# Optimization experiments

Hardware: AMD Instinct MI355X
Metric: run time of the kernel (lower is better)

## Reference

```python
import jax, jax.numpy as jnp
import numpy as np
from jax import lax

T, I, H, L = 4096, 101, 1000, 4  # seq len, letters_num, hidden, num_layers


def setup_inputs() -> dict:
    key = jax.random.key(0)
    ks = jax.random.split(key, 9)
    s = 0.03  # weight scale ~ 1/sqrt(H)
    return {
        "x": jax.random.normal(ks[0], (T, 1, I), jnp.float32),
        "enc_Wih": jax.random.normal(ks[1], (L, 4 * H, I), jnp.float32) * s,
        "enc_Whh": jax.random.normal(ks[2], (L, 4 * H, H), jnp.float32) * s,
        "enc_bih": jax.random.normal(ks[3], (L, 4 * H), jnp.float32) * s,
        "enc_bhh": jax.random.normal(ks[4], (L, 4 * H), jnp.float32) * s,
        "dec_Wih": jax.random.normal(ks[5], (L, 4 * I, H), jnp.float32) * s,
        "dec_Whh": jax.random.normal(ks[6], (L, 4 * I, I), jnp.float32) * s,
        "dec_bih": jax.random.normal(ks[7], (L, 4 * I), jnp.float32) * s,
        "dec_bhh": jax.random.normal(ks[8], (L, 4 * I), jnp.float32) * s,
        "length": T,
    }


def _lstm_cell(x, h, c, Wih, Whh, bih, bhh):
    # PyTorch LSTMCell gate order: i, f, g, o
    gates = x @ Wih.T + bih + h @ Whh.T + bhh  # [T, 4*Hout]
    i, f, g, o = jnp.split(gates, 4, axis=-1)
    c = jax.nn.sigmoid(f) * c + jax.nn.sigmoid(i) * jnp.tanh(g)
    h = jax.nn.sigmoid(o) * jnp.tanh(c)
    return h, c


def _stack(xt, Wih, Whh, bih, bhh, hout):
    # Hidden is reset per timestep in the original, so timesteps are a batch;
    # only the layer chain is sequential. Every layer consumes the same xt.
    t = xt.shape[0]
    init = (jnp.zeros((t, hout), xt.dtype), jnp.zeros((t, hout), xt.dtype))

    def body(carry, p):
        h, c = carry
        wih, whh, bi, bh = p
        h, c = _lstm_cell(xt, h, c, wih, whh, bi, bh)
        return (h, c), None

    (h, _), _ = lax.scan(body, init, (Wih, Whh, bih, bhh))
    return h


def reference(x, enc_Wih, enc_Whh, enc_bih, enc_bhh,
              dec_Wih, dec_Whh, dec_bih, dec_bhh, length):
    xt = x[:, 0, :]                      # [T, I]
    hdim = enc_Whh.shape[-1]
    odim = dec_Whh.shape[-1]
    enc = jax.nn.relu(_stack(xt, enc_Wih, enc_Whh, enc_bih, enc_bhh, hdim))  # [T, H]
    dec = _stack(enc, dec_Wih, dec_Whh, dec_bih, dec_bhh, odim)              # [T, O]
    out = jax.nn.log_softmax(dec, axis=-1)[:, None, :]                       # [T, 1, O]
    return out
```

## Files before the change

kernel.cpp:

```cpp
#include <hip/hip_runtime.h>
#include <cstdint>
#include <cstddef>
#include <cmath>

typedef __bf16 bf16_t;
typedef __bf16 bf16x8 __attribute__((ext_vector_type(8)));
typedef float floatx4 __attribute__((ext_vector_type(4)));

#define AS1 __attribute__((address_space(1)))
#define AS3 __attribute__((address_space(3)))

__device__ __forceinline__ void gload_lds16(const bf16_t* g, bf16_t* l) {
    __builtin_amdgcn_global_load_lds((AS1 void*)(uintptr_t)(g), (AS3 void*)(l), 16, 0, 0);
}

__device__ __forceinline__ float sigf(float x) { return 1.0f / (1.0f + __expf(-x)); }
__device__ __forceinline__ float tanhfast(float x) { return 1.0f - 2.0f / (__expf(2.0f * x) + 1.0f); }

template<int BM>
__global__ __launch_bounds__(256, 4)
void gemm_lstm(const bf16_t* __restrict__ A, const bf16_t* __restrict__ B,
               const float* __restrict__ bias,
               const float* __restrict__ zp, float* __restrict__ zout, int ldZ,
               float* __restrict__ c, int EP,
               bf16_t* __restrict__ hb, int ldH, int hoff, float* __restrict__ hf,
               int K, int ldA, int ldB, int relu, int czero)
{
    constexpr int AI = BM / 32;
    __shared__ bf16_t As[BM * 64];
    __shared__ bf16_t Bs[128 * 64];
    const int tid  = threadIdx.x;
    const int lane = tid & 63;
    const int w    = tid >> 6;
    const int wm   = (w & 1) * (BM / 2);
    const int wn   = (w >> 1) * 64;
    const int m0   = blockIdx.y * BM;
    const int n0   = blockIdx.x * 128;

    floatx4 zero = {0.0f, 0.0f, 0.0f, 0.0f};
    floatx4 acc[AI][4];
#pragma unroll
    for (int i = 0; i < AI; ++i)
#pragma unroll
        for (int j = 0; j < 4; ++j) acc[i][j] = zero;

    const int srow = lane >> 3;
    const int sk   = ((lane & 7) ^ srow) * 8;
    const int fr   = lane & 15;
    const int fx   = fr & 7;

    const bf16_t* Ag = A + (size_t)(m0 + srow) * ldA + sk;
    const bf16_t* Bg = B + (size_t)(n0 + srow) * ldB + sk;

    for (int k0 = 0; k0 < K; k0 += 64) {
        __syncthreads();
#pragma unroll
        for (int j = 0; j < AI; ++j) {
            int r0 = (w * AI + j) * 8;
            gload_lds16(Ag + (size_t)r0 * ldA + k0, As + r0 * 64 + lane * 8);
        }
#pragma unroll
        for (int j = 0; j < 4; ++j) {
            int r0 = (w * 4 + j) * 8;
            gload_lds16(Bg + (size_t)r0 * ldB + k0, Bs + r0 * 64 + lane * 8);
        }
        __syncthreads();
#pragma unroll
        for (int kk = 0; kk < 64; kk += 32) {
            const int pc = ((((kk >> 3) + (lane >> 4)) ^ fx) << 3);
            bf16x8 af[AI], bfr[4];
#pragma unroll
            for (int i = 0; i < AI; ++i)
                af[i] = *(const bf16x8*)(As + (wm + i * 16 + fr) * 64 + pc);
#pragma unroll
            for (int j = 0; j < 4; ++j)
                bfr[j] = *(const bf16x8*)(Bs + (wn + j * 16 + fr) * 64 + pc);
#pragma unroll
            for (int i = 0; i < AI; ++i)
#pragma unroll
                for (int j = 0; j < 4; ++j)
                    acc[i][j] = __builtin_amdgcn_mfma_f32_16x16x32_bf16(af[i], bfr[j], acc[i][j], 0, 0, 0);
        }
    }

    const int crow = (lane >> 4) * 4;
    const int ccol = lane & 15;
    const int nn   = n0 + wn;

    if (zout) {
        float bi[4];
#pragma unroll
        for (int j = 0; j < 4; ++j) bi[j] = bias[nn + j * 16 + ccol];
#pragma unroll
        for (int i = 0; i < AI; ++i) {
#pragma unroll
            for (int r = 0; r < 4; ++r) {
                int t = m0 + wm + i * 16 + crow + r;
                float* zr = zout + (size_t)t * ldZ + nn + ccol;
#pragma unroll
                for (int j = 0; j < 4; ++j) zr[j * 16] = acc[i][j][r] + bi[j];
            }
        }
        return;
    }

    const int e = (nn >> 2) + ccol;
    float bi[4];
    if (!zp) {
#pragma unroll
        for (int j = 0; j < 4; ++j) bi[j] = bias[nn + j * 16 + ccol];
    }

#pragma unroll
    for (int i = 0; i < AI; ++i) {
#pragma unroll
        for (int r = 0; r < 4; ++r) {
            int t = m0 + wm + i * 16 + crow + r;
            float g0, g1, g2, g3;
            if (zp) {
                const float* zr = zp + (size_t)t * ldZ + nn + ccol;
                g0 = acc[i][0][r] + zr[0];
                g1 = acc[i][1][r] + zr[16];
                g2 = acc[i][2][r] + zr[32];
                g3 = acc[i][3][r] + zr[48];
            } else {
                g0 = acc[i][0][r] + bi[0];
                g1 = acc[i][1][r] + bi[1];
                g2 = acc[i][2][r] + bi[2];
                g3 = acc[i][3][r] + bi[3];
            }
            size_t cix = (size_t)t * EP + e;
            float cold = 0.0f;
            if (!czero) cold = c[cix];
            float cv = sigf(g1) * cold + sigf(g0) * tanhfast(g2);
            c[cix] = cv;
            float hv = sigf(g3) * tanhfast(cv);
            if (relu) hv = fmaxf(hv, 0.0f);
            if (hb) hb[(size_t)t * ldH + hoff + e] = (bf16_t)hv;
            else    hf[(size_t)t * EP + e] = hv;
        }
    }
}

__global__ void pack_all(const float* __restrict__ x,
                         const float* __restrict__ eWih, const float* __restrict__ eWhh,
                         const float* __restrict__ ebih, const float* __restrict__ ebhh,
                         const float* __restrict__ dWih, const float* __restrict__ dWhh,
                         const float* __restrict__ dbih, const float* __restrict__ dbhh,
                         bf16_t* __restrict__ Aenc, bf16_t* __restrict__ Wenc,
                         bf16_t* __restrict__ Wdec,
                         float* __restrict__ bse, float* __restrict__ bsd)
{
    const int b = blockIdx.x;
    if (b < 9216) {
        int gid = b * 256 + threadIdx.x;
        int row = gid / 144, grp = gid - row * 144;
        int l = row >> 12, p = row & 4095;
        int g = (p >> 4) & 3, e = ((p >> 6) << 4) + (p & 15);
        int c0 = grp * 8;
        float v[8];
#pragma unroll
        for (int u = 0; u < 8; ++u) v[u] = 0.0f;
        if (e < 1000) {
            size_t r = (size_t)l * 4000 + g * 1000 + e;
            if (c0 >= 128 && c0 < 1128) {
                const float* src = eWhh + r * 1000 + (c0 - 128);
                float4 a = *(const float4*)src;
                float4 bq = *(const float4*)(src + 4);
                v[0]=a.x; v[1]=a.y; v[2]=a.z; v[3]=a.w; v[4]=bq.x; v[5]=bq.y; v[6]=bq.z; v[7]=bq.w;
            } else if (c0 < 128) {
                const float* src = eWih + r * 101;
#pragma unroll
                for (int u = 0; u < 8; ++u) { int cc = c0 + u; if (cc < 101) v[u] = src[cc]; }
            }
        }
        bf16x8 o;
#pragma unroll
        for (int u = 0; u < 8; ++u) o[u] = (bf16_t)v[u];
        *(bf16x8*)(Wenc + (size_t)row * 1152 + c0) = o;
    } else if (b < 11520) {
        int gid = (b - 9216) * 256 + threadIdx.x;
        int row = gid / 144, grp = gid - row * 144;
        int c0  = grp * 8;
        float v[8];
#pragma unroll
        for (int u = 0; u < 8; ++u) v[u] = 0.0f;
        if (c0 < 101) {
            const float* src = x + (size_t)row * 101;
#pragma unroll
            for (int u = 0; u < 8; ++u) { int cc = c0 + u; if (cc < 101) v[u] = src[cc]; }
        }
        bf16x8 o;
#pragma unroll
        for (int u = 0; u < 8; ++u) o[u] = (bf16_t)v[u];
        *(bf16x8*)(Aenc + (size_t)row * 1152 + c0) = o;
    } else if (b < 12672) {
        int gid = (b - 11520) * 256 + threadIdx.x;
        int row = gid / 144, grp = gid - row * 144;
        int l = row >> 9, p = row & 511;
        int g = (p >> 4) & 3, e = ((p >> 6) << 4) + (p & 15);
        int c0 = grp * 8;
        float v[8];
#pragma unroll
        for (int u = 0; u < 8; ++u) v[u] = 0.0f;
        if (e < 101) {
            size_t r = (size_t)l * 404 + g * 101 + e;
            if (c0 < 1000) {
                const float* src = dWih + r * 1000 + c0;
                float4 a = *(const float4*)src;
                float4 bq = *(const float4*)(src + 4);
                v[0]=a.x; v[1]=a.y; v[2]=a.z; v[3]=a.w; v[4]=bq.x; v[5]=bq.y; v[6]=bq.z; v[7]=bq.w;
            } else if (c0 >= 1024 && c0 < 1128) {
                const float* src = dWhh + r * 101;
#pragma unroll
                for (int u = 0; u < 8; ++u) { int cc = c0 + u; if (cc < 1125) v[u] = src[cc - 1024]; }
            }
        }
        bf16x8 o;
#pragma unroll
        for (int u = 0; u < 8; ++u) o[u] = (bf16_t)v[u];
        *(bf16x8*)(Wdec + (size_t)row * 1152 + c0) = o;
    } else {
        int idx = (b - 12672) * 256 + threadIdx.x;
        if (idx < 16384) {
            int l = idx >> 12, p = idx & 4095;
            int g = (p >> 4) & 3, e = ((p >> 6) << 4) + (p & 15);
            bse[idx] = (e < 1000) ? (ebih[l * 4000 + g * 1000 + e] + ebhh[l * 4000 + g * 1000 + e]) : 0.0f;
        } else {
            int k = idx - 16384;
            int l = k >> 9, p = k & 511;
            int g = (p >> 4) & 3, e = ((p >> 6) << 4) + (p & 15);
            bsd[k] = (e < 101) ? (dbih[l * 404 + g * 101 + e] + dbhh[l * 404 + g * 101 + e]) : 0.0f;
        }
    }
}

__global__ void log_softmax_k(const float* __restrict__ h, float* __restrict__ out)
{
    int row = blockIdx.x;
    int l   = threadIdx.x;
    const float* hr = h + (size_t)row * 128;
    float v1 = (l < 101)      ? hr[l]      : -INFINITY;
    float v2 = (l + 64 < 101) ? hr[l + 64] : -INFINITY;
    float m = fmaxf(v1, v2);
#pragma unroll
    for (int off = 32; off > 0; off >>= 1) m = fmaxf(m, __shfl_down(m, off));
    m = __shfl(m, 0);
    float ev = ((l < 101) ? __expf(v1 - m) : 0.0f) + ((l + 64 < 101) ? __expf(v2 - m) : 0.0f);
#pragma unroll
    for (int off = 32; off > 0; off >>= 1) ev += __shfl_down(ev, off);
    float lse = m + __logf(__shfl(ev, 0));
    float* orow = out + (size_t)row * 101;
    if (l < 101)      orow[l]      = v1 - lse;
    if (l + 64 < 101) orow[l + 64] = v2 - lse;
}

extern "C" void kernel_launch(void* const* d_in, const int* in_sizes, int n_in,
                              void* d_out, int out_size, void* d_ws, size_t ws_size,
                              hipStream_t stream)
{
    (void)in_sizes; (void)n_in; (void)out_size; (void)ws_size;
    const float* x    = (const float*)d_in[0];
    const float* eWih = (const float*)d_in[1];
    const float* eWhh = (const float*)d_in[2];
    const float* ebih = (const float*)d_in[3];
    const float* ebhh = (const float*)d_in[4];
    const float* dWih = (const float*)d_in[5];
    const float* dWhh = (const float*)d_in[6];
    const float* dbih = (const float*)d_in[7];
    const float* dbhh = (const float*)d_in[8];

    char* ws = (char*)d_ws;
    bf16_t* Aenc = (bf16_t*)(ws);
    bf16_t* Wenc = (bf16_t*)(ws + 9437184);
    bf16_t* Adec = (bf16_t*)(ws + 47185920);
    bf16_t* Wdec = (bf16_t*)(ws + 56623104);
    float*  bse  = (float*) (ws + 61341696);
    float*  bsd  = (float*) (ws + 61407232);
    float*  cenc = (float*) (ws + 61415424);
    float*  cdec = (float*) (ws + 78192640);
    float*  hdec = (float*) (ws + 80289792);
    float*  Z    = (float*)(ws + 9437184);

    pack_all<<<12744, 256, 0, stream>>>(x, eWih, eWhh, ebih, ebhh, dWih, dWhh, dbih, dbhh,
                                        Aenc, Wenc, Wdec, bse, bsd);

    for (int l = 0; l < 4; ++l) {
        gemm_lstm<128><<<dim3(32, 32), 256, 0, stream>>>(
            Aenc, Wenc + (size_t)l * 4096 * 1152, bse + l * 4096,
            nullptr, nullptr, 0,
            cenc, 1024,
            (l < 3) ? Aenc : Adec, 1152, (l < 3) ? 128 : 0, nullptr,
            (l == 0) ? 128 : 1152, 1152, 1152, (l == 3) ? 1 : 0, (l == 0) ? 1 : 0);
    }

    gemm_lstm<128><<<dim3(16, 32), 256, 0, stream>>>(
        Adec, Wdec, bsd,
        nullptr, Z, 2048,
        nullptr, 0,
        nullptr, 0, 0, nullptr,
        1024, 1152, 1152, 0, 0);

    for (int l = 0; l < 4; ++l) {
        gemm_lstm<32><<<dim3(4, 128), 256, 0, stream>>>(
            Adec + 1024, Wdec + 1024, bsd + l * 512,
            Z + l * 512, nullptr, 2048,
            cdec, 128,
            (l < 3) ? Adec : nullptr, 1152, 1024, (l == 3) ? hdec : nullptr,
            (l == 0) ? 0 : 128, 1152, 1152, 0, (l == 0) ? 1 : 0);
    }
    log_softmax_k<<<4096, 64, 0, stream>>>(hdec, (float*)d_out);
}
```

Measured before the change: 339.3 us.

## Fuse decoder LSTM layers and log-softmax into a single kernel

Replaces the four per-layer decoder GEMM+LSTM launches and the separate log_softmax launch with one kernel. Each block handles 16 timesteps across all four decoder layers. The cell state stays in registers and the hidden state in LDS, and log-softmax runs at the end. This removes launch overhead and the global-memory traffic for c and h between layers. The cost is low parallelism (256 blocks) and recurrent weights read directly from global memory without LDS staging.

```diff
diff --git a/kernel.cpp b/kernel.cpp
--- a/kernel.cpp
+++ b/kernel.cpp
@@ -21,9 +21,9 @@
 __global__ __launch_bounds__(256, 4)
 void gemm_lstm(const bf16_t* __restrict__ A, const bf16_t* __restrict__ B,
                const float* __restrict__ bias,
-               const float* __restrict__ zp, float* __restrict__ zout, int ldZ,
+               float* __restrict__ zout, int ldZ,
                float* __restrict__ c, int EP,
-               bf16_t* __restrict__ hb, int ldH, int hoff, float* __restrict__ hf,
+               bf16_t* __restrict__ hb, int ldH, int hoff,
                int K, int ldA, int ldB, int relu, int czero)
 {
     constexpr int AI = BM / 32;
@@ -86,11 +86,11 @@
     const int crow = (lane >> 4) * 4;
     const int ccol = lane & 15;
     const int nn   = n0 + wn;
+    float bi[4];
+#pragma unroll
+    for (int j = 0; j < 4; ++j) bi[j] = bias[nn + j * 16 + ccol];
 
     if (zout) {
-        float bi[4];
-#pragma unroll
-        for (int j = 0; j < 4; ++j) bi[j] = bias[nn + j * 16 + ccol];
 #pragma unroll
         for (int i = 0; i < AI; ++i) {
 #pragma unroll
@@ -105,30 +105,15 @@
     }
 
     const int e = (nn >> 2) + ccol;
-    float bi[4];
-    if (!zp) {
-#pragma unroll
-        for (int j = 0; j < 4; ++j) bi[j] = bias[nn + j * 16 + ccol];
-    }
-
 #pragma unroll
     for (int i = 0; i < AI; ++i) {
 #pragma unroll
         for (int r = 0; r < 4; ++r) {
             int t = m0 + wm + i * 16 + crow + r;
-            float g0, g1, g2, g3;
-            if (zp) {
-                const float* zr = zp + (size_t)t * ldZ + nn + ccol;
-                g0 = acc[i][0][r] + zr[0];
-                g1 = acc[i][1][r] + zr[16];
-                g2 = acc[i][2][r] + zr[32];
-                g3 = acc[i][3][r] + zr[48];
-            } else {
-                g0 = acc[i][0][r] + bi[0];
-                g1 = acc[i][1][r] + bi[1];
-                g2 = acc[i][2][r] + bi[2];
-                g3 = acc[i][3][r] + bi[3];
-            }
+            float g0 = acc[i][0][r] + bi[0];
+            float g1 = acc[i][1][r] + bi[1];
+            float g2 = acc[i][2][r] + bi[2];
+            float g3 = acc[i][3][r] + bi[3];
             size_t cix = (size_t)t * EP + e;
             float cold = 0.0f;
             if (!czero) cold = c[cix];
@@ -136,9 +121,91 @@
             c[cix] = cv;
             float hv = sigf(g3) * tanhfast(cv);
             if (relu) hv = fmaxf(hv, 0.0f);
-            if (hb) hb[(size_t)t * ldH + hoff + e] = (bf16_t)hv;
-            else    hf[(size_t)t * EP + e] = hv;
-        }
+            hb[(size_t)t * ldH + hoff + e] = (bf16_t)hv;
+        }
+    }
+}
+
+__global__ __launch_bounds__(256)
+void dec_fused(const float* __restrict__ Z, const bf16_t* __restrict__ Wd,
+               float* __restrict__ out)
+{
+    __shared__ bf16_t hB[16 * 136];
+    __shared__ float  hS[16 * 132];
+    const int tid  = threadIdx.x;
+    const int lane = tid & 63;
+    const int w    = tid >> 6;
+    const int m0   = blockIdx.x * 16;
+    const int ccol = lane & 15;
+    const int crow = (lane >> 4) * 4;
+    const int ksl  = (lane >> 4) * 8;
+
+    float cst[2][4];
+    floatx4 zerov = {0.0f, 0.0f, 0.0f, 0.0f};
+
+    for (int l = 0; l < 4; ++l) {
+        floatx4 acc[2][4];
+#pragma unroll
+        for (int q = 0; q < 2; ++q)
+#pragma unroll
+            for (int g = 0; g < 4; ++g) acc[q][g] = zerov;
+
+        if (l > 0) {
+#pragma unroll
+            for (int kk = 0; kk < 128; kk += 32) {
+                bf16x8 a = *(const bf16x8*)(hB + ccol * 136 + kk + ksl);
+#pragma unroll
+                for (int j = 0; j < 8; ++j) {
+                    const bf16_t* wp = Wd + (size_t)(l * 512 + w * 128 + j * 16 + ccol) * 1152
+                                          + 1024 + kk + ksl;
+                    bf16x8 b = *(const bf16x8*)wp;
+                    acc[j >> 2][j & 3] =
+                        __builtin_amdgcn_mfma_f32_16x16x32_bf16(a, b, acc[j >> 2][j & 3], 0, 0, 0);
+                }
+            }
+        }
+        __syncthreads();
+
+#pragma unroll
+        for (int q = 0; q < 2; ++q) {
+#pragma unroll
+            for (int r = 0; r < 4; ++r) {
+                int t = m0 + crow + r;
+                const float* zr = Z + (size_t)t * 2048 + l * 512 + w * 128 + q * 64 + ccol;
+                float g0 = acc[q][0][r] + zr[0];
+                float g1 = acc[q][1][r] + zr[16];
+                float g2 = acc[q][2][r] + zr[32];
+                float g3 = acc[q][3][r] + zr[48];
+                float cold = (l == 0) ? 0.0f : cst[q][r];
+                float cv = sigf(g1) * cold + sigf(g0) * tanhfast(g2);
+                cst[q][r] = cv;
+                float hv = sigf(g3) * tanhfast(cv);
+                int e = w * 32 + q * 16 + ccol;
+                if (l < 3) hB[(crow + r) * 136 + e] = (bf16_t)hv;
+                else       hS[(crow + r) * 132 + e] = hv;
+            }
+        }
+        __syncthreads();
+    }
+
+#pragma unroll
+    for (int rr = 0; rr < 4; ++rr) {
+        int row = w * 4 + rr;
+        const float* hr = hS + row * 132;
+        float v1 = (lane < 101)      ? hr[lane]      : -INFINITY;
+        float v2 = (lane + 64 < 101) ? hr[lane + 64] : -INFINITY;
+        float m = fmaxf(v1, v2);
+#pragma unroll
+        for (int off = 32; off > 0; off >>= 1) m = fmaxf(m, __shfl_down(m, off));
+        m = __shfl(m, 0);
+        float ev = ((lane < 101) ? __expf(v1 - m) : 0.0f)
+                 + ((lane + 64 < 101) ? __expf(v2 - m) : 0.0f);
+#pragma unroll
+        for (int off = 32; off > 0; off >>= 1) ev += __shfl_down(ev, off);
+        float lse = m + __logf(__shfl(ev, 0));
+        float* orow = out + (size_t)(m0 + row) * 101;
+        if (lane < 101)      orow[lane]      = v1 - lse;
+        if (lane + 64 < 101) orow[lane + 64] = v2 - lse;
     }
 }
 
@@ -235,26 +302,6 @@
     }
 }
 
-__global__ void log_softmax_k(const float* __restrict__ h, float* __restrict__ out)
-{
-    int row = blockIdx.x;
-    int l   = threadIdx.x;
-    const float* hr = h + (size_t)row * 128;
-    float v1 = (l < 101)      ? hr[l]      : -INFINITY;
-    float v2 = (l + 64 < 101) ? hr[l + 64] : -INFINITY;
-    float m = fmaxf(v1, v2);
-#pragma unroll
-    for (int off = 32; off > 0; off >>= 1) m = fmaxf(m, __shfl_down(m, off));
-    m = __shfl(m, 0);
-    float ev = ((l < 101) ? __expf(v1 - m) : 0.0f) + ((l + 64 < 101) ? __expf(v2 - m) : 0.0f);
-#pragma unroll
-    for (int off = 32; off > 0; off >>= 1) ev += __shfl_down(ev, off);
-    float lse = m + __logf(__shfl(ev, 0));
-    float* orow = out + (size_t)row * 101;
-    if (l < 101)      orow[l]      = v1 - lse;
-    if (l + 64 < 101) orow[l + 64] = v2 - lse;
-}
-
 extern "C" void kernel_launch(void* const* d_in, const int* in_sizes, int n_in,
                               void* d_out, int out_size, void* d_ws, size_t ws_size,
                               hipStream_t stream)
@@ -278,8 +325,6 @@
     float*  bse  = (float*) (ws + 61341696);
     float*  bsd  = (float*) (ws + 61407232);
     float*  cenc = (float*) (ws + 61415424);
-    float*  cdec = (float*) (ws + 78192640);
-    float*  hdec = (float*) (ws + 80289792);
     float*  Z    = (float*)(ws + 9437184);
 
     pack_all<<<12744, 256, 0, stream>>>(x, eWih, eWhh, ebih, ebhh, dWih, dWhh, dbih, dbhh,
@@ -288,26 +333,18 @@
     for (int l = 0; l < 4; ++l) {
         gemm_lstm<128><<<dim3(32, 32), 256, 0, stream>>>(
             Aenc, Wenc + (size_t)l * 4096 * 1152, bse + l * 4096,
-            nullptr, nullptr, 0,
+            nullptr, 0,
             cenc, 1024,
-            (l < 3) ? Aenc : Adec, 1152, (l < 3) ? 128 : 0, nullptr,
+            (l < 3) ? Aenc : Adec, 1152, (l < 3) ? 128 : 0,
             (l == 0) ? 128 : 1152, 1152, 1152, (l == 3) ? 1 : 0, (l == 0) ? 1 : 0);
     }
 
     gemm_lstm<128><<<dim3(16, 32), 256, 0, stream>>>(
         Adec, Wdec, bsd,
-        nullptr, Z, 2048,
+        Z, 2048,
         nullptr, 0,
-        nullptr, 0, 0, nullptr,
+        nullptr, 0, 0,
         1024, 1152, 1152, 0, 0);
 
-    for (int l = 0; l < 4; ++l) {
-        gemm_lstm<32><<<dim3(4, 128), 256, 0, stream>>>(
-            Adec + 1024, Wdec + 1024, bsd + l * 512,
-            Z + l * 512, nullptr, 2048,
-            cdec, 128,
-            (l < 3) ? Adec : nullptr, 1152, 1024, (l == 3) ? hdec : nullptr,
-            (l == 0) ? 0 : 128, 1152, 1152, 0, (l == 0) ? 1 : 0);
-    }
-    log_softmax_k<<<4096, 64, 0, stream>>>(hdec, (float*)d_out);
-}
+    dec_fused<<<256, 256, 0, stream>>>(Z, Wdec, (float*)d_out);
+}
```

Result: no change. 342.8 us (+1.0%).
